# Optimization experiments

Measured on AMD Instinct MI355X. Metric: run time of the kernel, lower is better.

The kernel has to match this reference:

```python
import jax, jax.numpy as jnp
import numpy as np

GELU = lambda v: jax.nn.gelu(v, approximate=False)  # torch nn.GELU default (exact erf)


def _gconv(x, w):
    # grouped conv1d, valid padding; w: (C,1,K), groups=C. lax conv = cross-correlation, same as torch.
    return jax.lax.conv_general_dilated(x, w, (1,), [(0, 0)],
                                        dimension_numbers=('NCH', 'OIH', 'NCH'),
                                        feature_group_count=x.shape[1])


def _conv(x, w, b):
    # dense conv1d, kernel 3, padding=1
    y = jax.lax.conv_general_dilated(x, w, (1,), [(1, 1)],
                                     dimension_numbers=('NCH', 'OIH', 'NCH'))
    return y + b[None, :, None]


def setup_inputs() -> dict:
    key = jax.random.key(0)
    ks = jax.random.split(key, 12)
    B, C, L = 8, 64, 2048
    H, FL, HD, TD, level = 32, 8, 64, 16, 3
    Cs = (1 + level) * C  # 256 channels into the ODE
    n = lambda k, s: (jax.random.normal(k, s) * 0.05).astype(jnp.float32)
    z = lambda s: jnp.zeros(s, jnp.float32)
    return dict(
        x=jax.random.normal(ks[0], (B, C, L), jnp.float32),
        # DyWAN_QR params
        sw1=n(ks[1], (H, C)), sb1=z((H,)),
        sw2=n(ks[2], (H, H)), sb2=z((H,)),
        sw3=n(ks[3], (2 * FL, H)), sb3=z((2 * FL,)),
        # ODE time embed / FiLM params
        tw1=n(ks[4], (TD, 1)), tb1=z((TD,)),
        tw2=n(ks[5], (TD, TD)), tb2=z((TD,)),
        cw=n(ks[6], (2 * HD, TD)), cb=z((2 * HD,)),
        # ODE conv stack params
        k1=n(ks[7], (HD, Cs, 3)), kb1=z((HD,)),
        k2=n(ks[8], (HD, HD, 3)), kb2=z((HD,)),
        k3=n(ks[9], (Cs, HD, 3)), kb3=z((Cs,)),
    )


def reference(x, sw1, sb1, sw2, sb2, sw3, sb3, tw1, tb1, tw2, tb2, cw, cb,
              k1, kb1, k2, kb2, k3, kb3):
    B, C, L = x.shape
    level, FL, T = 3, 8, 5

    def dywan(a):
        # stat_net: adaptive max pool over L -> (B,C) -> Linear -> GELU
        feat = GELU(jnp.max(a, axis=-1) @ sw1.T + sb1)
        raw = GELU(feat @ sw2.T + sb2) @ sw3.T + sb3  # (B, 2*FL)
        lo_raw, hi_raw = raw[:, :FL], raw[:, FL:]
        # QR of an (FL,1) column vector == L2 normalization (up to LAPACK sign)
        lo = lo_raw / jnp.linalg.norm(lo_raw, axis=1, keepdims=True)
        hi = hi_raw / jnp.linalg.norm(hi_raw, axis=1, keepdims=True)
        return lo, hi

    pad = FL - 1
    coeffs = [x]
    approx = x
    for _ in range(level):
        lo, hi = dywan(approx)
        lo_f = jnp.broadcast_to(lo.mean(0)[None, None, :], (C, 1, FL))
        hi_f = jnp.broadcast_to(hi.mean(0)[None, None, :], (C, 1, FL))
        ap = jnp.pad(approx, ((0, 0), (0, 0), (pad // 2, pad - pad // 2)), mode='reflect')
        new_approx = _gconv(ap, lo_f)[..., :L]
        coeffs.append(_gconv(ap, hi_f)[..., :L])
        approx = new_approx
    stacked = jnp.concatenate(coeffs, axis=1)  # (B, (1+level)*C, L)

    def ode_f(t, y):
        te = jnp.reshape(t, (1, 1)).astype(y.dtype)
        te = GELU(te @ tw1.T + tb1) @ tw2.T + tb2          # (1, TD)
        cond = te @ cw.T + cb                               # (1, 2*HD)
        hd = cond.shape[1] // 2
        gamma, beta = cond[:, :hd], cond[:, hd:]
        h = _conv(y, k1, kb1)
        h = (1.0 + gamma[:, :, None]) * h + beta[:, :, None]  # FiLM
        h = GELU(h)
        h = GELU(_conv(h, k2, kb2))
        return _conv(h, k3, kb3)

    # dopri5 tableau, fixed grid over linspace(0, 1, T) (b7 = 0, so 6 stages)
    hs = 1.0 / (T - 1)
    y = stacked
    for i in range(T - 1):
        t0 = i * hs
        s1 = ode_f(t0, y)
        s2 = ode_f(t0 + hs / 5, y + hs * (1 / 5) * s1)
        s3 = ode_f(t0 + 3 * hs / 10, y + hs * (3 / 40 * s1 + 9 / 40 * s2))
        s4 = ode_f(t0 + 4 * hs / 5, y + hs * (44 / 45 * s1 - 56 / 15 * s2 + 32 / 9 * s3))
        s5 = ode_f(t0 + 8 * hs / 9, y + hs * (19372 / 6561 * s1 - 25360 / 2187 * s2
                                              + 64448 / 6561 * s3 - 212 / 729 * s4))
        s6 = ode_f(t0 + hs, y + hs * (9017 / 3168 * s1 - 355 / 33 * s2 + 46732 / 5247 * s3
                                      + 49 / 176 * s4 - 5103 / 18656 * s5))
        y = y + hs * (35 / 384 * s1 + 500 / 1113 * s3 + 125 / 192 * s4
                      - 2187 / 6784 * s5 + 11 / 84 * s6)
    ode_out = y

    yl = ode_out[:, :C, :]
    yh0 = ode_out[:, C:2 * C, :]
    yh1 = ode_out[:, 2 * C:3 * C, :]
    yh2 = ode_out[:, 3 * C:4 * C, :]

    dx = ode_f(jnp.float32(1.0), ode_out)
    inner = jnp.sum(stacked * dx, axis=(1, 2))  # (B,)
    ecloss = jnp.mean(inner ** 2)
    return (yl, yh0, yh1, yh2, ecloss)
```

## Files before the change

### kernel.cpp

```cpp
#include <hip/hip_runtime.h>
#include <math.h>

#define B 8
#define C 64
#define L 2048
#define CS 256
#define BCL  (B*C*L)
#define BCSL (B*CS*L)
#define HS 0.25f

typedef unsigned short u16;
typedef unsigned int   u32;
typedef __attribute__((ext_vector_type(8))) short sh8;
typedef __attribute__((ext_vector_type(4))) float f4;
typedef __attribute__((ext_vector_type(8))) unsigned short us8;
typedef __attribute__((ext_vector_type(4))) unsigned short us4;

__device__ __forceinline__ float gelu(float x) {
    return 0.5f * x * (1.0f + erff(x * 0.70710678118654752440f));
}
__device__ __forceinline__ u16 f2b(float f) {
    u32 u = __float_as_uint(f);
    u32 r = u + 0x7FFFu + ((u >> 16) & 1u);
    return (u16)(r >> 16);
}
__device__ __forceinline__ float b2f(u16 h) {
    return __uint_as_float(((u32)h) << 16);
}

struct ComboB { const u16* p[6]; float c[6]; };

__global__ __launch_bounds__(256) void prep_k(const float* __restrict__ w,
        u16* __restrict__ dst, int IC, int OC) {
    int idx = blockIdx.x * 256 + threadIdx.x;
    int OCG = OC >> 4;
    int j = idx & 7, lane = (idx >> 3) & 63, t = idx >> 9;
    int ocg = t % OCG, c = t / OCG;
    int oc = ocg * 16 + (lane & 15);
    int K = c * 32 + ((lane >> 4) & 3) * 8 + j;
    int kk = K / IC, ic = K % IC;
    dst[idx] = f2b(w[((size_t)oc * IC + ic) * 3 + kk]);
}

__global__ void cond25_k(const float* __restrict__ tw1, const float* __restrict__ tb1,
                         const float* __restrict__ tw2, const float* __restrict__ tb2,
                         const float* __restrict__ cw, const float* __restrict__ cb,
                         float* __restrict__ condall) {
    __shared__ float te1[16], te2[16];
    int tix = blockIdx.x;
    int tid = threadIdx.x;
    double add[6] = {0.0, 0.25/5.0, 3.0*0.25/10.0, 4.0*0.25/5.0, 8.0*0.25/9.0, 0.25};
    float t = (tix == 24) ? 1.0f : (float)((double)(tix / 6) * 0.25 + add[tix % 6]);
    if (tid < 16) te1[tid] = gelu(t * tw1[tid] + tb1[tid]);
    __syncthreads();
    if (tid < 16) {
        float s = tb2[tid];
        for (int k = 0; k < 16; ++k) s += te1[k] * tw2[tid*16+k];
        te2[tid] = s;
    }
    __syncthreads();
    float s = cb[tid];
    for (int j = 0; j < 16; ++j) s += te2[j] * cw[tid*16+j];
    condall[tix*128 + tid] = s;
}

template<int NC, int EPI>
__global__ __launch_bounds__(256) void fused_k(ComboB in,
        const u16* __restrict__ wp1, const float* __restrict__ kb1,
        const u16* __restrict__ wp2, const float* __restrict__ kb2,
        const u16* __restrict__ wp3, const float* __restrict__ kb3,
        const float* __restrict__ condall, int tix,
        u16* __restrict__ outSb,
        float* __restrict__ y, u16* __restrict__ yb,
        float* __restrict__ outp, const float* __restrict__ stacked,
        double* __restrict__ inner)
{
    __shared__ u16 xs1[34][264];
    __shared__ u16 h1t[34][72];
    __shared__ u16 h2t[18][72];
    __shared__ u16 ypart[16][264];
    __shared__ double sred[4];
    const int tid = threadIdx.x;
    const int l0  = blockIdx.x * 16;
    const int b   = blockIdx.y;
    const int g0  = l0 - 3;

    const float cy1 = HS*(35.f/384.f), cy3 = HS*(500.f/1113.f),
                cy4 = HS*(125.f/192.f), cy5 = -HS*(2187.f/6784.f),
                cy6 = HS*(11.f/84.f);

    for (int i = tid; i < 12*264; i += 256) xs1[22 + i/264][i%264] = 0;
    if (tid < 144) h1t[32 + tid/72][tid%72] = 0;

    for (int idx = tid; idx < 22*32; idx += 256) {
        int r = idx >> 5, c8 = idx & 31;
        int gl = g0 + r;
        us8 val;
        if (gl >= 0 && gl < L) {
            size_t a = ((size_t)b * L + gl) * 256 + c8 * 8;
            us8 v0 = *(const us8*)(in.p[0] + a);
            if (NC == 1) {
                val = v0;
            } else {
                float f[8];
                float yp[8];
                #pragma unroll
                for (int j = 0; j < 8; ++j) { f[j] = b2f(v0[j]); yp[j] = 0.f; }
                #pragma unroll
                for (int t = 1; t < NC; ++t) {
                    us8 vt = *(const us8*)(in.p[t] + a);
                    #pragma unroll
                    for (int j = 0; j < 8; ++j) {
                        float bv = b2f(vt[j]);
                        f[j] += in.c[t] * bv;
                        if ((EPI == 1 || EPI == 2) && (t == 1 || t == 3 || t == 4 || t == 5)) {
                            float cy = (t == 1) ? cy1 : (t == 3) ? cy3 : (t == 4) ? cy4 : cy5;
                            yp[j] += cy * bv;
                        }
                    }
                }
                #pragma unroll
                for (int j = 0; j < 8; ++j) val[j] = f2b(f[j]);
                if ((EPI == 1 || EPI == 2) && r >= 3 && r < 19) {
                    us8 ypk;
                    #pragma unroll
                    for (int j = 0; j < 8; ++j) ypk[j] = f2b(yp[j]);
                    *(us8*)&ypart[r - 3][c8 * 8] = ypk;
                }
            }
        } else {
            #pragma unroll
            for (int j = 0; j < 8; ++j) val[j] = 0;
        }
        *(us8*)&xs1[r][c8 * 8] = val;
    }
    __syncthreads();

    const int wave = tid >> 6, lane = tid & 63;
    const int nlo = lane & 15, quad = lane >> 4;

    f4 a1[2];
    a1[0] = f4{0.f,0.f,0.f,0.f}; a1[1] = a1[0];
    {
        const sh8* w1 = (const sh8*)wp1;
        for (int c = 0; c < 24; ++c) {
            int kk = c >> 3, ic0 = (c & 7) << 5;
            sh8 A = w1[(c*4 + wave)*64 + lane];
            #pragma unroll
            for (int nf = 0; nf < 2; ++nf) {
                sh8 Bv = *(const sh8*)&xs1[nf*16 + nlo + kk][ic0 + quad*8];
                a1[nf] = __builtin_amdgcn_mfma_f32_16x16x32_bf16(A, Bv, a1[nf], 0, 0, 0);
            }
        }
    }
    {
        const float* cd = condall + tix*128;
        #pragma unroll
        for (int nf = 0; nf < 2; ++nf) {
            int p = nf*16 + nlo;
            int gp = l0 - 2 + p;
            bool ok = (p < 20) && (gp >= 0) && (gp < L);
            #pragma unroll
            for (int reg = 0; reg < 4; ++reg) {
                int oc = wave*16 + quad*4 + reg;
                float v = (1.f + cd[oc]) * (a1[nf][reg] + kb1[oc]) + cd[64+oc];
                h1t[p][oc] = ok ? f2b(gelu(v)) : (u16)0;
            }
        }
    }
    __syncthreads();

    f4 a2[2];
    a2[0] = f4{0.f,0.f,0.f,0.f}; a2[1] = a2[0];
    {
        const sh8* w2 = (const sh8*)wp2;
        #pragma unroll
        for (int c = 0; c < 6; ++c) {
            int kk = c >> 1, ic0 = (c & 1) << 5;
            sh8 A = w2[(c*4 + wave)*64 + lane];
            #pragma unroll
            for (int nf = 0; nf < 2; ++nf) {
                sh8 Bv = *(const sh8*)&h1t[nf*16 + nlo + kk][ic0 + quad*8];
                a2[nf] = __builtin_amdgcn_mfma_f32_16x16x32_bf16(A, Bv, a2[nf], 0, 0, 0);
            }
        }
    }
    {
        #pragma unroll
        for (int nf = 0; nf < 2; ++nf) {
            int q = nf*16 + nlo;
            if (q < 18) {
                int gq = l0 - 1 + q;
                bool ok = (gq >= 0) && (gq < L);
                #pragma unroll
                for (int reg = 0; reg < 4; ++reg) {
                    int oc = wave*16 + quad*4 + reg;
                    h2t[q][oc] = ok ? f2b(gelu(a2[nf][reg] + kb2[oc])) : (u16)0;
                }
            }
        }
    }
    __syncthreads();

    f4 a3[4];
    #pragma unroll
    for (int mf = 0; mf < 4; ++mf) a3[mf] = f4{0.f,0.f,0.f,0.f};
    {
        const sh8* w3 = (const sh8*)wp3;
        #pragma unroll
        for (int c = 0; c < 6; ++c) {
            int kk = c >> 1, ic0 = (c & 1) << 5;
            sh8 B0 = *(const sh8*)&h2t[nlo + kk][ic0 + quad*8];
            #pragma unroll
            for (int mf = 0; mf < 4; ++mf) {
                sh8 A = w3[(c*16 + wave*4 + mf)*64 + lane];
                a3[mf] = __builtin_amdgcn_mfma_f32_16x16x32_bf16(A, B0, a3[mf], 0, 0, 0);
            }
        }
    }

    const int pos = l0 + nlo;
    if (EPI == 3) {
        double acc = 0.0;
        #pragma unroll
        for (int mf = 0; mf < 4; ++mf)
            #pragma unroll
            for (int reg = 0; reg < 4; ++reg) {
                int oc = (wave*4 + mf)*16 + quad*4 + reg;
                size_t idx = ((size_t)b*CS + oc)*L + pos;
                float dx = a3[mf][reg] + kb3[oc];
                acc += (double)stacked[idx] * (double)dx;
            }
        #pragma unroll
        for (int off = 32; off > 0; off >>= 1) acc += __shfl_down(acc, off, 64);
        if (lane == 0) sred[wave] = acc;
        __syncthreads();
        if (tid == 0) atomicAdd(&inner[b], sred[0] + sred[1] + sred[2] + sred[3]);
    } else if (EPI == 0) {
        #pragma unroll
        for (int mf = 0; mf < 4; ++mf) {
            int baseoc = (wave*4 + mf)*16 + quad*4;
            us4 pk;
            #pragma unroll
            for (int reg = 0; reg < 4; ++reg)
                pk[reg] = f2b(a3[mf][reg] + kb3[baseoc + reg]);
            *(us4*)(outSb + ((size_t)b*L + pos)*256 + baseoc) = pk;
        }
    } else {
        #pragma unroll
        for (int mf = 0; mf < 4; ++mf) {
            int baseoc = (wave*4 + mf)*16 + quad*4;
            us4 yp4 = *(const us4*)&ypart[nlo][baseoc];
            us4 pk;
            #pragma unroll
            for (int reg = 0; reg < 4; ++reg) {
                int oc = baseoc + reg;
                size_t idx = ((size_t)b*CS + oc)*L + pos;
                float s6 = a3[mf][reg] + kb3[oc];
                float yv = y[idx] + b2f(yp4[reg]) + cy6 * s6;
                pk[reg] = f2b(yv);
                if (EPI == 1) y[idx] = yv;
                if (EPI == 2) {
                    size_t oidx = (((size_t)(oc >> 6)*B + b)*64 + (oc & 63))*L + pos;
                    outp[oidx] = yv;
                }
            }
            *(us4*)(yb + ((size_t)b*L + pos)*256 + baseoc) = pk;
        }
    }
}

__global__ __launch_bounds__(256) void rowmax_k(const float* __restrict__ a, float* __restrict__ bm) {
    __shared__ float red[256];
    int row = blockIdx.x;
    const float* p = a + (size_t)row * L;
    float m = -1e30f;
    for (int t = threadIdx.x; t < L; t += 256) m = fmaxf(m, p[t]);
    red[threadIdx.x] = m;
    __syncthreads();
    for (int s = 128; s > 0; s >>= 1) {
        if (threadIdx.x < s) red[threadIdx.x] = fmaxf(red[threadIdx.x], red[threadIdx.x + s]);
        __syncthreads();
    }
    if (threadIdx.x == 0) bm[row] = red[0];
}

__global__ __launch_bounds__(256) void mlp_k(const float* __restrict__ bm,
    const float* __restrict__ sw1, const float* __restrict__ sb1,
    const float* __restrict__ sw2, const float* __restrict__ sb2,
    const float* __restrict__ sw3, const float* __restrict__ sb3,
    float* __restrict__ filt) {
    __shared__ float m[8][64], f1[8][32], f2[8][32], raw[8][16], nrm[8][2];
    int tid = threadIdx.x;
    for (int i = tid; i < 512; i += 256) m[i >> 6][i & 63] = bm[i];
    __syncthreads();
    {
        int b = tid >> 5, h = tid & 31;
        float s = sb1[h];
        for (int c = 0; c < 64; ++c) s += m[b][c] * sw1[h*64+c];
        f1[b][h] = gelu(s);
    }
    __syncthreads();
    {
        int b = tid >> 5, h = tid & 31;
        float s = sb2[h];
        for (int k = 0; k < 32; ++k) s += f1[b][k] * sw2[h*32+k];
        f2[b][h] = gelu(s);
    }
    __syncthreads();
    if (tid < 128) {
        int b = tid >> 4, j = tid & 15;
        float s = sb3[j];
        for (int k = 0; k < 32; ++k) s += f2[b][k] * sw3[j*32+k];
        raw[b][j] = s;
    }
    __syncthreads();
    if (tid < 16) {
        int b = tid >> 1, half = tid & 1;
        float s = 0.f;
        for (int j = 0; j < 8; ++j) { float v = raw[b][half*8+j]; s += v*v; }
        nrm[b][half] = sqrtf(s);
    }
    __syncthreads();
    if (tid < 16) {
        int half = tid >> 3;
        float s = 0.f;
        for (int b = 0; b < 8; ++b) s += raw[b][tid] / nrm[b][half];
        filt[tid] = s * 0.125f;
    }
}

__global__ __launch_bounds__(256) void wconv_k(const float* __restrict__ ap,
    const float* __restrict__ filt, float* __restrict__ apOut,
    float* __restrict__ stacked, int lev) {
    __shared__ float f[16];
    if (threadIdx.x < 16) f[threadIdx.x] = filt[threadIdx.x];
    __syncthreads();
    size_t idx = (size_t)blockIdx.x * 256 + threadIdx.x;
    int l = (int)(idx & 2047);
    size_t bc = idx >> 11;
    int c = (int)(bc & 63), b = (int)(bc >> 6);
    const float* row = ap + (bc << 11);
    float lo = 0.f, hi = 0.f;
    #pragma unroll
    for (int k = 0; k < 8; ++k) {
        int mI = l + k - 3;
        mI = mI < 0 ? -mI : (mI >= L ? 2*L - 2 - mI : mI);
        float v = row[mI];
        lo += v * f[k];
        hi += v * f[8+k];
    }
    apOut[idx] = lo;
    stacked[((size_t)b * CS + (size_t)(lev+1) * 64 + c) * L + l] = hi;
}

__global__ __launch_bounds__(256) void copyx_k(const float* __restrict__ x, float* __restrict__ st) {
    size_t i = (size_t)blockIdx.x * 256 + threadIdx.x;
    size_t b = i >> 17, rem = i & 131071;
    st[b * ((size_t)CS*L) + rem] = x[i];
}

__global__ __launch_bounds__(256) void tinit_k(const float* __restrict__ st,
        float* __restrict__ y, u16* __restrict__ yb) {
    __shared__ float t[64][65];
    const int tid = threadIdx.x;
    const int l0 = blockIdx.x * 64, c0 = blockIdx.y * 64, b = blockIdx.z;
    #pragma unroll
    for (int k = 0; k < 16; ++k) {
        int c = k * 4 + (tid >> 6), l = tid & 63;
        size_t idx = ((size_t)b*CS + c0 + c) * L + l0 + l;
        float v = st[idx];
        y[idx] = v;
        t[c][l] = v;
    }
    __syncthreads();
    #pragma unroll
    for (int k = 0; k < 16; ++k) {
        int p = k * 4 + (tid >> 6), ch = tid & 63;
        yb[((size_t)b * L + l0 + p) * 256 + c0 + ch] = f2b(t[ch][p]);
    }
}

__global__ void ecfin_k(const double* __restrict__ inner, float* __restrict__ out) {
    double s = 0.0;
    for (int b = 0; b < 8; ++b) s += inner[b] * inner[b];
    out[BCSL] = (float)(s / 8.0);
}

extern "C" void kernel_launch(void* const* d_in, const int* in_sizes, int n_in,
                              void* d_out, int out_size, void* d_ws, size_t ws_size,
                              hipStream_t stream) {
    const float* x   = (const float*)d_in[0];
    const float* sw1 = (const float*)d_in[1];
    const float* sb1 = (const float*)d_in[2];
    const float* sw2 = (const float*)d_in[3];
    const float* sb2 = (const float*)d_in[4];
    const float* sw3 = (const float*)d_in[5];
    const float* sb3 = (const float*)d_in[6];
    const float* tw1 = (const float*)d_in[7];
    const float* tb1 = (const float*)d_in[8];
    const float* tw2 = (const float*)d_in[9];
    const float* tb2 = (const float*)d_in[10];
    const float* cw  = (const float*)d_in[11];
    const float* cb  = (const float*)d_in[12];
    const float* k1  = (const float*)d_in[13];
    const float* kb1 = (const float*)d_in[14];
    const float* k2  = (const float*)d_in[15];
    const float* kb2 = (const float*)d_in[16];
    const float* k3  = (const float*)d_in[17];
    const float* kb3 = (const float*)d_in[18];
    float* out = (float*)d_out;

    char* cur = (char*)d_ws;
    auto alloc = [&](size_t bytes) { void* p = cur; cur += (bytes + 255) & ~(size_t)255; return p; };
    float* stacked = (float*)alloc(BCSL * 4);
    float* y       = (float*)alloc(BCSL * 4);
    u16*   yb      = (u16*)  alloc(BCSL * 2);
    u16*   sbuf[5];
    for (int i = 0; i < 5; ++i) sbuf[i] = (u16*)alloc(BCSL * 2);
    float* cond  = (float*)alloc(3200 * 4);
    float* bmax  = (float*)alloc(512 * 4);
    float* filt  = (float*)alloc(16 * 4);
    double* inner = (double*)alloc(8 * 8);
    u16* wp1 = (u16*)alloc(49152 * 2);
    u16* wp2 = (u16*)alloc(12288 * 2);
    u16* wp3 = (u16*)alloc(49152 * 2);

    u16 *s1b = sbuf[0], *s2b = sbuf[1], *s3b = sbuf[2], *s4b = sbuf[3], *s5b = sbuf[4];

    hipMemsetAsync(inner, 0, 8 * sizeof(double), stream);

    prep_k<<<192, 256, 0, stream>>>(k1, wp1, CS, C);
    prep_k<<<48,  256, 0, stream>>>(k2, wp2, C,  C);
    prep_k<<<192, 256, 0, stream>>>(k3, wp3, C,  CS);
    cond25_k<<<25, 128, 0, stream>>>(tw1, tb1, tw2, tb2, cw, cb, cond);

    copyx_k<<<4096, 256, 0, stream>>>(x, stacked);
    const float* apIn = x;
    float* apBuf[2] = {(float*)s1b, (float*)s2b};
    for (int lev = 0; lev < 3; ++lev) {
        rowmax_k<<<512, 256, 0, stream>>>(apIn, bmax);
        mlp_k<<<1, 256, 0, stream>>>(bmax, sw1, sb1, sw2, sb2, sw3, sb3, filt);
        float* apOut = apBuf[lev & 1];
        wconv_k<<<4096, 256, 0, stream>>>(apIn, filt, apOut, stacked, lev);
        apIn = apOut;
    }
    tinit_k<<<dim3(32, 4, 8), 256, 0, stream>>>(stacked, y, yb);

    const float hs = HS;
    dim3 cg(128, 8);
    #define LAUNCH(NC, EPI, CIN, TIX, OUTSB, OUTP, STK) \
        fused_k<NC, EPI><<<cg, 256, 0, stream>>>(CIN, wp1, kb1, wp2, kb2, wp3, kb3, \
            cond, TIX, OUTSB, y, yb, OUTP, STK, inner)

    for (int i = 0; i < 4; ++i) {
        ComboB cA{}; cA.p[0] = yb;
        LAUNCH(1, 0, cA, i*6+0, s1b, nullptr, nullptr);

        ComboB cB{}; cB.p[0] = yb; cB.p[1] = s1b; cB.c[1] = hs*(1.f/5.f);
        LAUNCH(2, 0, cB, i*6+1, s2b, nullptr, nullptr);

        ComboB cC{}; cC.p[0] = yb;
        cC.p[1] = s1b; cC.c[1] = hs*(3.f/40.f);
        cC.p[2] = s2b; cC.c[2] = hs*(9.f/40.f);
        LAUNCH(3, 0, cC, i*6+2, s3b, nullptr, nullptr);

        ComboB cD{}; cD.p[0] = yb;
        cD.p[1] = s1b; cD.c[1] = hs*(44.f/45.f);
        cD.p[2] = s2b; cD.c[2] = -hs*(56.f/15.f);
        cD.p[3] = s3b; cD.c[3] = hs*(32.f/9.f);
        LAUNCH(4, 0, cD, i*6+3, s4b, nullptr, nullptr);

        ComboB cE{}; cE.p[0] = yb;
        cE.p[1] = s1b; cE.c[1] = hs*(19372.f/6561.f);
        cE.p[2] = s2b; cE.c[2] = -hs*(25360.f/2187.f);
        cE.p[3] = s3b; cE.c[3] = hs*(64448.f/6561.f);
        cE.p[4] = s4b; cE.c[4] = -hs*(212.f/729.f);
        LAUNCH(5, 0, cE, i*6+4, s5b, nullptr, nullptr);

        ComboB cF{}; cF.p[0] = yb;
        cF.p[1] = s1b; cF.c[1] = hs*(9017.f/3168.f);
        cF.p[2] = s2b; cF.c[2] = -hs*(355.f/33.f);
        cF.p[3] = s3b; cF.c[3] = hs*(46732.f/5247.f);
        cF.p[4] = s4b; cF.c[4] = hs*(49.f/176.f);
        cF.p[5] = s5b; cF.c[5] = -hs*(5103.f/18656.f);
        if (i < 3) {
            LAUNCH(6, 1, cF, i*6+5, nullptr, nullptr, nullptr);
        } else {
            LAUNCH(6, 2, cF, i*6+5, nullptr, out, nullptr);
        }
    }

    ComboB cZ{}; cZ.p[0] = yb;
    LAUNCH(1, 3, cZ, 24, nullptr, nullptr, stacked);
    ecfin_k<<<1, 1, 0, stream>>>(inner, out);
    #undef LAUNCH
}
```

Baseline: 712.0 us.

## Halve fused ODE tile to 8 positions, transpose y state, swizzle block order

Result: slower. 782.1 us (+9.8%).

```diff
diff --git a/kernel.cpp b/kernel.cpp
--- a/kernel.cpp
+++ b/kernel.cpp
@@ -65,138 +65,131 @@
 }
 
 template<int NC, int EPI>
-__global__ __launch_bounds__(256) void fused_k(ComboB in,
+__global__ __launch_bounds__(256, 8) void fused_k(ComboB in,
         const u16* __restrict__ wp1, const float* __restrict__ kb1,
         const u16* __restrict__ wp2, const float* __restrict__ kb2,
         const u16* __restrict__ wp3, const float* __restrict__ kb3,
         const float* __restrict__ condall, int tix,
         u16* __restrict__ outSb,
-        float* __restrict__ y, u16* __restrict__ yb,
+        float* __restrict__ ytr, u16* __restrict__ yb,
         float* __restrict__ outp, const float* __restrict__ stacked,
         double* __restrict__ inner)
 {
-    __shared__ u16 xs1[34][264];
-    __shared__ u16 h1t[34][72];
-    __shared__ u16 h2t[18][72];
-    __shared__ u16 ypart[16][264];
+    __shared__ u16 xs1[16][264];
+    __shared__ u16 h1t[12][72];
+    __shared__ u16 h2t[10][72];
+    __shared__ u16 ypart[8][264];
     __shared__ double sred[4];
     const int tid = threadIdx.x;
-    const int l0  = blockIdx.x * 16;
+    const int bx  = blockIdx.x;
+    const int tile = ((bx & 7) << 5) | (bx >> 3);
+    const int l0  = tile * 8;
     const int b   = blockIdx.y;
-    const int g0  = l0 - 3;
 
     const float cy1 = HS*(35.f/384.f), cy3 = HS*(500.f/1113.f),
                 cy4 = HS*(125.f/192.f), cy5 = -HS*(2187.f/6784.f),
                 cy6 = HS*(11.f/84.f);
 
-    for (int i = tid; i < 12*264; i += 256) xs1[22 + i/264][i%264] = 0;
-    if (tid < 144) h1t[32 + tid/72][tid%72] = 0;
-
-    for (int idx = tid; idx < 22*32; idx += 256) {
-        int r = idx >> 5, c8 = idx & 31;
-        int gl = g0 + r;
-        us8 val;
-        if (gl >= 0 && gl < L) {
-            size_t a = ((size_t)b * L + gl) * 256 + c8 * 8;
-            us8 v0 = *(const us8*)(in.p[0] + a);
-            if (NC == 1) {
-                val = v0;
-            } else {
-                float f[8];
-                float yp[8];
-                #pragma unroll
-                for (int j = 0; j < 8; ++j) { f[j] = b2f(v0[j]); yp[j] = 0.f; }
-                #pragma unroll
-                for (int t = 1; t < NC; ++t) {
-                    us8 vt = *(const us8*)(in.p[t] + a);
+    for (int i = tid; i < 264; i += 256) ((u32*)&xs1[14][0])[i] = 0;
+
+    #pragma unroll
+    for (int it = 0; it < 2; ++it) {
+        int idx = it * 256 + tid;
+        if (idx < 448) {
+            int r = idx >> 5, c8 = idx & 31;
+            int gl = l0 - 3 + r;
+            us8 val;
+            if (gl >= 0 && gl < L) {
+                size_t a = ((size_t)b * L + gl) * 256 + c8 * 8;
+                us8 v0 = *(const us8*)(in.p[0] + a);
+                if (NC == 1) {
+                    val = v0;
+                } else {
+                    float f[8], yp[8];
                     #pragma unroll
-                    for (int j = 0; j < 8; ++j) {
-                        float bv = b2f(vt[j]);
-                        f[j] += in.c[t] * bv;
-                        if ((EPI == 1 || EPI == 2) && (t == 1 || t == 3 || t == 4 || t == 5)) {
-                            float cy = (t == 1) ? cy1 : (t == 3) ? cy3 : (t == 4) ? cy4 : cy5;
-                            yp[j] += cy * bv;
+                    for (int j = 0; j < 8; ++j) { f[j] = b2f(v0[j]); yp[j] = 0.f; }
+                    #pragma unroll
+                    for (int t = 1; t < NC; ++t) {
+                        us8 vt = *(const us8*)(in.p[t] + a);
+                        #pragma unroll
+                        for (int j = 0; j < 8; ++j) {
+                            float bv = b2f(vt[j]);
+                            f[j] += in.c[t] * bv;
+                            if ((EPI == 1 || EPI == 2) && (t == 1 || t == 3 || t == 4 || t == 5)) {
+                                float cy = (t == 1) ? cy1 : (t == 3) ? cy3 : (t == 4) ? cy4 : cy5;
+                                yp[j] += cy * bv;
+                            }
                         }
                     }
+                    #pragma unroll
+                    for (int j = 0; j < 8; ++j) val[j] = f2b(f[j]);
+                    if ((EPI == 1 || EPI == 2) && r >= 3 && r < 11) {
+                        us8 ypk;
+                        #pragma unroll
+                        for (int j = 0; j < 8; ++j) ypk[j] = f2b(yp[j]);
+                        *(us8*)&ypart[r - 3][c8 * 8] = ypk;
+                    }
                 }
+            } else {
                 #pragma unroll
-                for (int j = 0; j < 8; ++j) val[j] = f2b(f[j]);
-                if ((EPI == 1 || EPI == 2) && r >= 3 && r < 19) {
-                    us8 ypk;
-                    #pragma unroll
-                    for (int j = 0; j < 8; ++j) ypk[j] = f2b(yp[j]);
-                    *(us8*)&ypart[r - 3][c8 * 8] = ypk;
-                }
+                for (int j = 0; j < 8; ++j) val[j] = 0;
             }
-        } else {
-            #pragma unroll
-            for (int j = 0; j < 8; ++j) val[j] = 0;
-        }
-        *(us8*)&xs1[r][c8 * 8] = val;
+            *(us8*)&xs1[r][c8 * 8] = val;
+        }
     }
     __syncthreads();
 
     const int wave = tid >> 6, lane = tid & 63;
     const int nlo = lane & 15, quad = lane >> 4;
 
-    f4 a1[2];
-    a1[0] = f4{0.f,0.f,0.f,0.f}; a1[1] = a1[0];
+    f4 a1 = {0.f,0.f,0.f,0.f};
     {
         const sh8* w1 = (const sh8*)wp1;
         for (int c = 0; c < 24; ++c) {
             int kk = c >> 3, ic0 = (c & 7) << 5;
             sh8 A = w1[(c*4 + wave)*64 + lane];
-            #pragma unroll
-            for (int nf = 0; nf < 2; ++nf) {
-                sh8 Bv = *(const sh8*)&xs1[nf*16 + nlo + kk][ic0 + quad*8];
-                a1[nf] = __builtin_amdgcn_mfma_f32_16x16x32_bf16(A, Bv, a1[nf], 0, 0, 0);
-            }
+            int row = nlo + kk; row = row > 15 ? 15 : row;
+            sh8 Bv = *(const sh8*)&xs1[row][ic0 + quad*8];
+            a1 = __builtin_amdgcn_mfma_f32_16x16x32_bf16(A, Bv, a1, 0, 0, 0);
         }
     }
     {
         const float* cd = condall + tix*128;
-        #pragma unroll
-        for (int nf = 0; nf < 2; ++nf) {
-            int p = nf*16 + nlo;
-            int gp = l0 - 2 + p;
-            bool ok = (p < 20) && (gp >= 0) && (gp < L);
+        int p = nlo;
+        int gp = l0 - 2 + p;
+        bool ok = (gp >= 0) && (gp < L);
+        if (p < 12) {
             #pragma unroll
             for (int reg = 0; reg < 4; ++reg) {
                 int oc = wave*16 + quad*4 + reg;
-                float v = (1.f + cd[oc]) * (a1[nf][reg] + kb1[oc]) + cd[64+oc];
+                float v = (1.f + cd[oc]) * (a1[reg] + kb1[oc]) + cd[64+oc];
                 h1t[p][oc] = ok ? f2b(gelu(v)) : (u16)0;
             }
         }
     }
     __syncthreads();
 
-    f4 a2[2];
-    a2[0] = f4{0.f,0.f,0.f,0.f}; a2[1] = a2[0];
+    f4 a2 = {0.f,0.f,0.f,0.f};
     {
         const sh8* w2 = (const sh8*)wp2;
         #pragma unroll
         for (int c = 0; c < 6; ++c) {
             int kk = c >> 1, ic0 = (c & 1) << 5;
             sh8 A = w2[(c*4 + wave)*64 + lane];
+            int row = nlo + kk; row = row > 11 ? 11 : row;
+            sh8 Bv = *(const sh8*)&h1t[row][ic0 + quad*8];
+            a2 = __builtin_amdgcn_mfma_f32_16x16x32_bf16(A, Bv, a2, 0, 0, 0);
+        }
+    }
+    {
+        int q = nlo;
+        int gq = l0 - 1 + q;
+        bool ok = (gq >= 0) && (gq < L);
+        if (q < 10) {
             #pragma unroll
-            for (int nf = 0; nf < 2; ++nf) {
-                sh8 Bv = *(const sh8*)&h1t[nf*16 + nlo + kk][ic0 + quad*8];
-                a2[nf] = __builtin_amdgcn_mfma_f32_16x16x32_bf16(A, Bv, a2[nf], 0, 0, 0);
-            }
-        }
-    }
-    {
-        #pragma unroll
-        for (int nf = 0; nf < 2; ++nf) {
-            int q = nf*16 + nlo;
-            if (q < 18) {
-                int gq = l0 - 1 + q;
-                bool ok = (gq >= 0) && (gq < L);
-                #pragma unroll
-                for (int reg = 0; reg < 4; ++reg) {
-                    int oc = wave*16 + quad*4 + reg;
-                    h2t[q][oc] = ok ? f2b(gelu(a2[nf][reg] + kb2[oc])) : (u16)0;
-                }
+            for (int reg = 0; reg < 4; ++reg) {
+                int oc = wave*16 + quad*4 + reg;
+                h2t[q][oc] = ok ? f2b(gelu(a2[reg] + kb2[oc])) : (u16)0;
             }
         }
     }
@@ -210,7 +203,8 @@
         #pragma unroll
         for (int c = 0; c < 6; ++c) {
             int kk = c >> 1, ic0 = (c & 1) << 5;
-            sh8 B0 = *(const sh8*)&h2t[nlo + kk][ic0 + quad*8];
+            int row = nlo + kk; row = row > 9 ? 9 : row;
+            sh8 B0 = *(const sh8*)&h2t[row][ic0 + quad*8];
             #pragma unroll
             for (int mf = 0; mf < 4; ++mf) {
                 sh8 A = w3[(c*16 + wave*4 + mf)*64 + lane];
@@ -222,50 +216,59 @@
     const int pos = l0 + nlo;
     if (EPI == 3) {
         double acc = 0.0;
-        #pragma unroll
-        for (int mf = 0; mf < 4; ++mf)
+        if (nlo < 8) {
             #pragma unroll
-            for (int reg = 0; reg < 4; ++reg) {
-                int oc = (wave*4 + mf)*16 + quad*4 + reg;
-                size_t idx = ((size_t)b*CS + oc)*L + pos;
-                float dx = a3[mf][reg] + kb3[oc];
-                acc += (double)stacked[idx] * (double)dx;
-            }
+            for (int mf = 0; mf < 4; ++mf)
+                #pragma unroll
+                for (int reg = 0; reg < 4; ++reg) {
+                    int oc = (wave*4 + mf)*16 + quad*4 + reg;
+                    size_t idx = ((size_t)b*CS + oc)*L + pos;
+                    float dx = a3[mf][reg] + kb3[oc];
+                    acc += (double)stacked[idx] * (double)dx;
+                }
+        }
         #pragma unroll
         for (int off = 32; off > 0; off >>= 1) acc += __shfl_down(acc, off, 64);
         if (lane == 0) sred[wave] = acc;
         __syncthreads();
         if (tid == 0) atomicAdd(&inner[b], sred[0] + sred[1] + sred[2] + sred[3]);
     } else if (EPI == 0) {
-        #pragma unroll
-        for (int mf = 0; mf < 4; ++mf) {
-            int baseoc = (wave*4 + mf)*16 + quad*4;
-            us4 pk;
+        if (nlo < 8) {
             #pragma unroll
-            for (int reg = 0; reg < 4; ++reg)
-                pk[reg] = f2b(a3[mf][reg] + kb3[baseoc + reg]);
-            *(us4*)(outSb + ((size_t)b*L + pos)*256 + baseoc) = pk;
+            for (int mf = 0; mf < 4; ++mf) {
+                int baseoc = (wave*4 + mf)*16 + quad*4;
+                us4 pk;
+                #pragma unroll
+                for (int reg = 0; reg < 4; ++reg)
+                    pk[reg] = f2b(a3[mf][reg] + kb3[baseoc + reg]);
+                *(us4*)(outSb + ((size_t)b*L + pos)*256 + baseoc) = pk;
+            }
         }
     } else {
-        #pragma unroll
-        for (int mf = 0; mf < 4; ++mf) {
-            int baseoc = (wave*4 + mf)*16 + quad*4;
-            us4 yp4 = *(const us4*)&ypart[nlo][baseoc];
-            us4 pk;
+        if (nlo < 8) {
             #pragma unroll
-            for (int reg = 0; reg < 4; ++reg) {
-                int oc = baseoc + reg;
-                size_t idx = ((size_t)b*CS + oc)*L + pos;
-                float s6 = a3[mf][reg] + kb3[oc];
-                float yv = y[idx] + b2f(yp4[reg]) + cy6 * s6;
-                pk[reg] = f2b(yv);
-                if (EPI == 1) y[idx] = yv;
-                if (EPI == 2) {
-                    size_t oidx = (((size_t)(oc >> 6)*B + b)*64 + (oc & 63))*L + pos;
-                    outp[oidx] = yv;
+            for (int mf = 0; mf < 4; ++mf) {
+                int baseoc = (wave*4 + mf)*16 + quad*4;
+                size_t ta = ((size_t)b*L + pos)*256 + baseoc;
+                us4 yp4 = *(const us4*)&ypart[nlo][baseoc];
+                f4 y4 = *(const f4*)(ytr + ta);
+                us4 pk;
+                f4 yo;
+                #pragma unroll
+                for (int reg = 0; reg < 4; ++reg) {
+                    int oc = baseoc + reg;
+                    float s6 = a3[mf][reg] + kb3[oc];
+                    float yv = y4[reg] + b2f(yp4[reg]) + cy6 * s6;
+                    yo[reg] = yv;
+                    pk[reg] = f2b(yv);
+                    if (EPI == 2) {
+                        size_t oidx = (((size_t)(oc >> 6)*B + b)*64 + (oc & 63))*L + pos;
+                        outp[oidx] = yv;
+                    }
                 }
+                if (EPI == 1) *(f4*)(ytr + ta) = yo;
+                *(us4*)(yb + ta) = pk;
             }
-            *(us4*)(yb + ((size_t)b*L + pos)*256 + baseoc) = pk;
         }
     }
 }
@@ -361,23 +364,23 @@
 }
 
 __global__ __launch_bounds__(256) void tinit_k(const float* __restrict__ st,
-        float* __restrict__ y, u16* __restrict__ yb) {
+        float* __restrict__ ytr, u16* __restrict__ yb) {
     __shared__ float t[64][65];
     const int tid = threadIdx.x;
     const int l0 = blockIdx.x * 64, c0 = blockIdx.y * 64, b = blockIdx.z;
     #pragma unroll
     for (int k = 0; k < 16; ++k) {
         int c = k * 4 + (tid >> 6), l = tid & 63;
-        size_t idx = ((size_t)b*CS + c0 + c) * L + l0 + l;
-        float v = st[idx];
-        y[idx] = v;
-        t[c][l] = v;
+        t[c][l] = st[((size_t)b*CS + c0 + c) * L + l0 + l];
     }
     __syncthreads();
     #pragma unroll
     for (int k = 0; k < 16; ++k) {
         int p = k * 4 + (tid >> 6), ch = tid & 63;
-        yb[((size_t)b * L + l0 + p) * 256 + c0 + ch] = f2b(t[ch][p]);
+        float v = t[ch][p];
+        size_t ta = ((size_t)b * L + l0 + p) * 256 + c0 + ch;
+        ytr[ta] = v;
+        yb[ta] = f2b(v);
     }
 }
 
@@ -414,7 +417,7 @@
     char* cur = (char*)d_ws;
     auto alloc = [&](size_t bytes) { void* p = cur; cur += (bytes + 255) & ~(size_t)255; return p; };
     float* stacked = (float*)alloc(BCSL * 4);
-    float* y       = (float*)alloc(BCSL * 4);
+    float* ytr     = (float*)alloc(BCSL * 4);
     u16*   yb      = (u16*)  alloc(BCSL * 2);
     u16*   sbuf[5];
     for (int i = 0; i < 5; ++i) sbuf[i] = (u16*)alloc(BCSL * 2);
@@ -445,13 +448,13 @@
         wconv_k<<<4096, 256, 0, stream>>>(apIn, filt, apOut, stacked, lev);
         apIn = apOut;
     }
-    tinit_k<<<dim3(32, 4, 8), 256, 0, stream>>>(stacked, y, yb);
+    tinit_k<<<dim3(32, 4, 8), 256, 0, stream>>>(stacked, ytr, yb);
 
     const float hs = HS;
-    dim3 cg(128, 8);
+    dim3 cg(256, 8);
     #define LAUNCH(NC, EPI, CIN, TIX, OUTSB, OUTP, STK) \
         fused_k<NC, EPI><<<cg, 256, 0, stream>>>(CIN, wp1, kb1, wp2, kb2, wp3, kb3, \
-            cond, TIX, OUTSB, y, yb, OUTP, STK, inner)
+            cond, TIX, OUTSB, ytr, yb, OUTP, STK, inner)
 
     for (int i = 0; i < 4; ++i) {
         ComboB cA{}; cA.p[0] = yb;
```

## Store fp32 ODE state channel-last and prefetch staged inputs into registers

Applied to the files above, without the earlier changes.

Result: no change. 725.5 us (+1.9%).

```diff
diff --git a/kernel.cpp b/kernel.cpp
--- a/kernel.cpp
+++ b/kernel.cpp
@@ -71,7 +71,7 @@
         const u16* __restrict__ wp3, const float* __restrict__ kb3,
         const float* __restrict__ condall, int tix,
         u16* __restrict__ outSb,
-        float* __restrict__ y, u16* __restrict__ yb,
+        float* __restrict__ ytr, u16* __restrict__ yb,
         float* __restrict__ outp, const float* __restrict__ stacked,
         double* __restrict__ inner)
 {
@@ -92,47 +92,77 @@
     for (int i = tid; i < 12*264; i += 256) xs1[22 + i/264][i%264] = 0;
     if (tid < 144) h1t[32 + tid/72][tid%72] = 0;
 
-    for (int idx = tid; idx < 22*32; idx += 256) {
-        int r = idx >> 5, c8 = idx & 31;
-        int gl = g0 + r;
-        us8 val;
-        if (gl >= 0 && gl < L) {
-            size_t a = ((size_t)b * L + gl) * 256 + c8 * 8;
-            us8 v0 = *(const us8*)(in.p[0] + a);
-            if (NC == 1) {
-                val = v0;
-            } else {
-                float f[8];
-                float yp[8];
-                #pragma unroll
-                for (int j = 0; j < 8; ++j) { f[j] = b2f(v0[j]); yp[j] = 0.f; }
-                #pragma unroll
-                for (int t = 1; t < NC; ++t) {
-                    us8 vt = *(const us8*)(in.p[t] + a);
+    {
+        constexpr int ITEMS = 22 * 32;
+        us8 rg[2][NC];
+        {
+            int idx = tid;
+            if (idx < ITEMS) {
+                int r = idx >> 5, c8 = idx & 31;
+                int gl = g0 + r;
+                if (gl >= 0 && gl < L) {
+                    size_t a = ((size_t)b * L + gl) * 256 + c8 * 8;
                     #pragma unroll
-                    for (int j = 0; j < 8; ++j) {
-                        float bv = b2f(vt[j]);
-                        f[j] += in.c[t] * bv;
-                        if ((EPI == 1 || EPI == 2) && (t == 1 || t == 3 || t == 4 || t == 5)) {
-                            float cy = (t == 1) ? cy1 : (t == 3) ? cy3 : (t == 4) ? cy4 : cy5;
-                            yp[j] += cy * bv;
+                    for (int t = 0; t < NC; ++t) rg[0][t] = *(const us8*)(in.p[t] + a);
+                }
+            }
+        }
+        #pragma unroll
+        for (int it = 0; it < 3; ++it) {
+            if (it < 2) {
+                int idx = (it + 1) * 256 + tid;
+                if (idx < ITEMS) {
+                    int r = idx >> 5, c8 = idx & 31;
+                    int gl = g0 + r;
+                    if (gl >= 0 && gl < L) {
+                        size_t a = ((size_t)b * L + gl) * 256 + c8 * 8;
+                        #pragma unroll
+                        for (int t = 0; t < NC; ++t)
+                            rg[(it + 1) & 1][t] = *(const us8*)(in.p[t] + a);
+                    }
+                }
+            }
+            int idx = it * 256 + tid;
+            if (idx < ITEMS) {
+                int r = idx >> 5, c8 = idx & 31;
+                int gl = g0 + r;
+                us8 val;
+                if (gl >= 0 && gl < L) {
+                    us8* R = rg[it & 1];
+                    if (NC == 1) {
+                        val = R[0];
+                    } else {
+                        float f[8], yp[8];
+                        #pragma unroll
+                        for (int j = 0; j < 8; ++j) { f[j] = b2f(R[0][j]); yp[j] = 0.f; }
+                        #pragma unroll
+                        for (int t = 1; t < NC; ++t) {
+                            #pragma unroll
+                            for (int j = 0; j < 8; ++j) {
+                                float bv = b2f(R[t][j]);
+                                f[j] += in.c[t] * bv;
+                                if ((EPI == 1 || EPI == 2) && (t == 1 || t == 3 || t == 4 || t == 5)) {
+                                    float cy = (t == 1) ? cy1 : (t == 3) ? cy3 : (t == 4) ? cy4 : cy5;
+                                    yp[j] += cy * bv;
+                                }
+                            }
+                        }
+                        #pragma unroll
+                        for (int j = 0; j < 8; ++j) val[j] = f2b(f[j]);
+                        if ((EPI == 1 || EPI == 2) && r >= 3 && r < 19) {
+                            us8 ypk;
+                            #pragma unroll
+                            for (int j = 0; j < 8; ++j) ypk[j] = f2b(yp[j]);
+                            *(us8*)&ypart[r - 3][c8 * 8] = ypk;
                         }
                     }
+                } else {
+                    #pragma unroll
+                    for (int j = 0; j < 8; ++j) val[j] = 0;
                 }
-                #pragma unroll
-                for (int j = 0; j < 8; ++j) val[j] = f2b(f[j]);
-                if ((EPI == 1 || EPI == 2) && r >= 3 && r < 19) {
-                    us8 ypk;
-                    #pragma unroll
-                    for (int j = 0; j < 8; ++j) ypk[j] = f2b(yp[j]);
-                    *(us8*)&ypart[r - 3][c8 * 8] = ypk;
-                }
-            }
-        } else {
-            #pragma unroll
-            for (int j = 0; j < 8; ++j) val[j] = 0;
-        }
-        *(us8*)&xs1[r][c8 * 8] = val;
+                *(us8*)&xs1[r][c8 * 8] = val;
+            }
+        }
     }
     __syncthreads();
 
@@ -250,22 +280,25 @@
         #pragma unroll
         for (int mf = 0; mf < 4; ++mf) {
             int baseoc = (wave*4 + mf)*16 + quad*4;
+            size_t ta = ((size_t)b*L + pos)*256 + baseoc;
             us4 yp4 = *(const us4*)&ypart[nlo][baseoc];
+            f4 y4 = *(const f4*)(ytr + ta);
             us4 pk;
+            f4 yo;
             #pragma unroll
             for (int reg = 0; reg < 4; ++reg) {
                 int oc = baseoc + reg;
-                size_t idx = ((size_t)b*CS + oc)*L + pos;
                 float s6 = a3[mf][reg] + kb3[oc];
-                float yv = y[idx] + b2f(yp4[reg]) + cy6 * s6;
+                float yv = y4[reg] + b2f(yp4[reg]) + cy6 * s6;
+                yo[reg] = yv;
                 pk[reg] = f2b(yv);
-                if (EPI == 1) y[idx] = yv;
                 if (EPI == 2) {
                     size_t oidx = (((size_t)(oc >> 6)*B + b)*64 + (oc & 63))*L + pos;
                     outp[oidx] = yv;
                 }
             }
-            *(us4*)(yb + ((size_t)b*L + pos)*256 + baseoc) = pk;
+            if (EPI == 1) *(f4*)(ytr + ta) = yo;
+            *(us4*)(yb + ta) = pk;
         }
     }
 }
@@ -361,23 +394,23 @@
 }
 
 __global__ __launch_bounds__(256) void tinit_k(const float* __restrict__ st,
-        float* __restrict__ y, u16* __restrict__ yb) {
+        float* __restrict__ ytr, u16* __restrict__ yb) {
     __shared__ float t[64][65];
     const int tid = threadIdx.x;
     const int l0 = blockIdx.x * 64, c0 = blockIdx.y * 64, b = blockIdx.z;
     #pragma unroll
     for (int k = 0; k < 16; ++k) {
         int c = k * 4 + (tid >> 6), l = tid & 63;
-        size_t idx = ((size_t)b*CS + c0 + c) * L + l0 + l;
-        float v = st[idx];
-        y[idx] = v;
-        t[c][l] = v;
+        t[c][l] = st[((size_t)b*CS + c0 + c) * L + l0 + l];
     }
     __syncthreads();
     #pragma unroll
     for (int k = 0; k < 16; ++k) {
         int p = k * 4 + (tid >> 6), ch = tid & 63;
-        yb[((size_t)b * L + l0 + p) * 256 + c0 + ch] = f2b(t[ch][p]);
+        float v = t[ch][p];
+        size_t ta = ((size_t)b * L + l0 + p) * 256 + c0 + ch;
+        ytr[ta] = v;
+        yb[ta] = f2b(v);
     }
 }
 
@@ -414,7 +447,7 @@
     char* cur = (char*)d_ws;
     auto alloc = [&](size_t bytes) { void* p = cur; cur += (bytes + 255) & ~(size_t)255; return p; };
     float* stacked = (float*)alloc(BCSL * 4);
-    float* y       = (float*)alloc(BCSL * 4);
+    float* ytr     = (float*)alloc(BCSL * 4);
     u16*   yb      = (u16*)  alloc(BCSL * 2);
     u16*   sbuf[5];
     for (int i = 0; i < 5; ++i) sbuf[i] = (u16*)alloc(BCSL * 2);
@@ -445,13 +478,13 @@
         wconv_k<<<4096, 256, 0, stream>>>(apIn, filt, apOut, stacked, lev);
         apIn = apOut;
     }
-    tinit_k<<<dim3(32, 4, 8), 256, 0, stream>>>(stacked, y, yb);
+    tinit_k<<<dim3(32, 4, 8), 256, 0, stream>>>(stacked, ytr, yb);
 
     const float hs = HS;
     dim3 cg(128, 8);
     #define LAUNCH(NC, EPI, CIN, TIX, OUTSB, OUTP, STK) \
         fused_k<NC, EPI><<<cg, 256, 0, stream>>>(CIN, wp1, kb1, wp2, kb2, wp3, kb3, \
-            cond, TIX, OUTSB, y, yb, OUTP, STK, inner)
+            cond, TIX, OUTSB, ytr, yb, OUTP, STK, inner)
 
     for (int i = 0; i < 4; ++i) {
         ComboB cA{}; cA.p[0] = yb;
```
